# Optimization experiments

Measured on AMD Instinct MI355X. Metric: run time of the kernel, lower is better.

## Reference

```python
import jax, jax.numpy as jnp
import numpy as np
from jax import lax

D = 1024      # d_model
NH = 16       # n_head
CA = 384      # adapter_channels
T = 16        # num_frames
B = 4         # videos
L = 257       # tokens = 16*16 patches + CLS
HW = 16       # spatial side


def setup_inputs() -> dict:
    key = jax.random.key(0)
    ks = jax.random.split(key, 12)
    s = 0.02
    f = lambda k, shp: jax.random.normal(k, shp, jnp.float32) * s
    return {
        'x': jax.random.normal(ks[0], (B * T, L, D), jnp.float32),
        'ln1_g': jnp.ones((D,), jnp.float32), 'ln1_b': jnp.zeros((D,), jnp.float32),
        'w_in': f(ks[1], (3 * D, D)), 'b_in': jnp.zeros((3 * D,), jnp.float32),
        'w_out': f(ks[2], (D, D)), 'b_out': jnp.zeros((D,), jnp.float32),
        'o_fc1_w': f(ks[3], (CA, D)), 'o_fc1_b': jnp.zeros((CA,), jnp.float32),
        'o_conv_w': f(ks[4], (3, 3, 1, CA)), 'o_conv_b': jnp.zeros((CA,), jnp.float32),
        'o_fc2_w': f(ks[5], (D, CA)), 'o_fc2_b': jnp.zeros((D,), jnp.float32),
        'a_fc1_w': f(ks[6], (CA, D)), 'a_fc1_b': jnp.zeros((CA,), jnp.float32),
        'a_conv_w': f(ks[7], (3, 1, CA)), 'a_conv_b': jnp.zeros((CA,), jnp.float32),
        'a_fc2_w': f(ks[8], (D, CA)), 'a_fc2_b': jnp.zeros((D,), jnp.float32),
        'ln2_g': jnp.ones((D,), jnp.float32), 'ln2_b': jnp.zeros((D,), jnp.float32),
        'mlp_fc_w': f(ks[9], (4 * D, D)), 'mlp_fc_b': jnp.zeros((4 * D,), jnp.float32),
        'mlp_proj_w': f(ks[10], (D, 4 * D)), 'mlp_proj_b': jnp.zeros((D,), jnp.float32),
    }


def _ln(x, g, b):
    # fp32 LayerNorm (matches CLIP LayerNorm subclass)
    x32 = x.astype(jnp.float32)
    mu = jnp.mean(x32, -1, keepdims=True)
    var = jnp.mean(jnp.square(x32 - mu), -1, keepdims=True)
    return ((x32 - mu) * lax.rsqrt(var + 1e-5) * g + b).astype(x.dtype)


def _mha(x, w_in, b_in, w_out, b_out):
    BT, Lq, C = x.shape
    hd = C // NH
    qkv = x @ w_in.T + b_in                       # (BT, L, 3C)
    q, k, v = jnp.split(qkv, 3, axis=-1)
    sh = lambda t: t.reshape(BT, Lq, NH, hd).transpose(0, 2, 1, 3)  # (BT, H, L, hd)
    q, k, v = sh(q), sh(k), sh(v)
    scores = jnp.einsum('bhqd,bhkd->bhqk', q * (hd ** -0.5), k)
    attn = jax.nn.softmax(scores, axis=-1)
    out = jnp.einsum('bhqk,bhkd->bhqd', attn, v)
    out = out.transpose(0, 2, 1, 3).reshape(BT, Lq, C)
    return out @ w_out.T + b_out


def _offset_adapter(x, fc1_w, fc1_b, conv_w, conv_b, fc2_w, fc2_b):
    BT, Lx, C = x.shape
    Bv = BT // T
    xs = x[:, 1:, :].reshape(Bv, T, Lx - 1, C)          # drop CLS
    former = jnp.concatenate([xs[:, :1], xs[:, :-1]], axis=1)
    off = xs - former                                    # temporal diff
    off = off @ fc1_w.T + fc1_b                          # (B, T, HW*HW, Ca)
    off = off.reshape(Bv * T, HW, HW, CA)
    # depthwise (1,3,3) Conv3d: kernel size 1 along T -> per-frame 3x3 depthwise conv
    off = lax.conv_general_dilated(off, conv_w, (1, 1), [(1, 1), (1, 1)],
                                   dimension_numbers=('NHWC', 'HWIO', 'NHWC'),
                                   feature_group_count=CA) + conv_b
    off = off.reshape(BT, Lx - 1, CA)
    return off @ fc2_w.T + fc2_b                         # (BT, L-1, C)


def _adapter2(x, a_fc1_w, a_fc1_b, a_conv_w, a_conv_b, a_fc2_w, a_fc2_b,
              o_fc1_w, o_fc1_b, o_conv_w, o_conv_b, o_fc2_w, o_fc2_b):
    BT, Lx, C = x.shape
    Bv = BT // T
    off = _offset_adapter(x, o_fc1_w, o_fc1_b, o_conv_w, o_conv_b, o_fc2_w, o_fc2_b)
    y = x @ a_fc1_w.T + a_fc1_b                          # (BT, L, Ca)
    y = y.reshape(Bv, T, Lx, CA).transpose(0, 2, 1, 3).reshape(Bv * Lx, T, CA)
    # depthwise Conv1d along the temporal axis
    y = lax.conv_general_dilated(y, a_conv_w, (1,), [(1, 1)],
                                 dimension_numbers=('NWC', 'WIO', 'NWC'),
                                 feature_group_count=CA) + a_conv_b
    y = y.reshape(Bv, Lx, T, CA).transpose(0, 2, 1, 3).reshape(BT, Lx, CA)
    y = y @ a_fc2_w.T + a_fc2_b                          # (BT, L, C)
    x_id = x.at[:, 1:, :].add(off)
    return y + x_id


def _block(x, ln1_g, ln1_b, w_in, b_in, w_out, b_out,
           a_fc1_w, a_fc1_b, a_conv_w, a_conv_b, a_fc2_w, a_fc2_b,
           o_fc1_w, o_fc1_b, o_conv_w, o_conv_b, o_fc2_w, o_fc2_b,
           ln2_g, ln2_b, mlp_fc_w, mlp_fc_b, mlp_proj_w, mlp_proj_b):
    x = x + _mha(_ln(x, ln1_g, ln1_b), w_in, b_in, w_out, b_out)
    x = _adapter2(x, a_fc1_w, a_fc1_b, a_conv_w, a_conv_b, a_fc2_w, a_fc2_b,
                  o_fc1_w, o_fc1_b, o_conv_w, o_conv_b, o_fc2_w, o_fc2_b)
    h = _ln(x, ln2_g, ln2_b) @ mlp_fc_w.T + mlp_fc_b
    h = h * jax.nn.sigmoid(1.702 * h)                    # QuickGELU
    return x + h @ mlp_proj_w.T + mlp_proj_b


def reference(x, ln1_g, ln1_b, w_in, b_in, w_out, b_out,
              o_fc1_w, o_fc1_b, o_conv_w, o_conv_b, o_fc2_w, o_fc2_b,
              a_fc1_w, a_fc1_b, a_conv_w, a_conv_b, a_fc2_w, a_fc2_b,
              ln2_g, ln2_b, mlp_fc_w, mlp_fc_b, mlp_proj_w, mlp_proj_b):
    return _block(x, ln1_g, ln1_b, w_in, b_in, w_out, b_out,
                  a_fc1_w, a_fc1_b, a_conv_w, a_conv_b, a_fc2_w, a_fc2_b,
                  o_fc1_w, o_fc1_b, o_conv_w, o_conv_b, o_fc2_w, o_fc2_b,
                  ln2_g, ln2_b, mlp_fc_w, mlp_fc_b, mlp_proj_w, mlp_proj_b)
```

## Files before the change

kernel.cpp:

```cpp
#include <hip/hip_runtime.h>
#include <cstdint>
#include <cstddef>


typedef unsigned short u16;
typedef __attribute__((ext_vector_type(4))) float  f32x4;
typedef __attribute__((ext_vector_type(8))) short  bf16x8;
typedef __attribute__((ext_vector_type(4))) unsigned int u32x4;

#define AS1 __attribute__((address_space(1)))
#define AS3 __attribute__((address_space(3)))

__device__ __forceinline__ float bf2f(u16 u) {
  unsigned int x = ((unsigned int)u) << 16;
  return __builtin_bit_cast(float, x);
}
__device__ __forceinline__ u16 f2bf(float f) {
  unsigned int x = __builtin_bit_cast(unsigned int, f);
  x = x + 0x7fffu + ((x >> 16) & 1u);
  return (u16)(x >> 16);
}
__device__ __forceinline__ unsigned int pack2(float a, float b) {
  return (unsigned int)f2bf(a) | ((unsigned int)f2bf(b) << 16);
}

__device__ __forceinline__ void gload_lds16(const void* g, void* l) {
  __builtin_amdgcn_global_load_lds((const AS1 unsigned int*)g,
                                   (AS3 unsigned int*)l, 16, 0, 0);
}

__global__ __launch_bounds__(256) void cvt_weights(
    const float* __restrict__ w_in, const float* __restrict__ w_out,
    const float* __restrict__ ofc1, const float* __restrict__ ofc2,
    const float* __restrict__ afc1, const float* __restrict__ afc2,
    const float* __restrict__ mfc,  const float* __restrict__ mproj,
    u16* __restrict__ dst)
{
  long i4 = (long)blockIdx.x * 256 + threadIdx.x;
  long e = i4 * 4;
  const float* src; long base;
  if      (e < 3145728L) { src = w_in;  base = 0L; }
  else if (e < 4194304L) { src = w_out; base = 3145728L; }
  else if (e < 4587520L) { src = ofc1;  base = 4194304L; }
  else if (e < 4980736L) { src = ofc2;  base = 4587520L; }
  else if (e < 5373952L) { src = afc1;  base = 4980736L; }
  else if (e < 5767168L) { src = afc2;  base = 5373952L; }
  else if (e < 9961472L) { src = mfc;   base = 5767168L; }
  else                   { src = mproj; base = 9961472L; }
  float4 v = *(const float4*)(src + (e - base));
  uint2 o; o.x = pack2(v.x, v.y); o.y = pack2(v.z, v.w);
  *(uint2*)(dst + e) = o;
}

__global__ __launch_bounds__(256) void ln_bf16(
    const float* __restrict__ x, const float* __restrict__ g,
    const float* __restrict__ b, u16* __restrict__ out)
{
  int row = blockIdx.x;
  const float4* xr = (const float4*)(x + (size_t)row * 1024);
  float4 v = xr[threadIdx.x];
  float s = v.x + v.y + v.z + v.w;
  float q = v.x * v.x + v.y * v.y + v.z * v.z + v.w * v.w;
  #pragma unroll
  for (int m = 1; m < 64; m <<= 1) { s += __shfl_xor(s, m); q += __shfl_xor(q, m); }
  __shared__ float ss[4], qq[4];
  if ((threadIdx.x & 63) == 0) { ss[threadIdx.x >> 6] = s; qq[threadIdx.x >> 6] = q; }
  __syncthreads();
  s = ss[0] + ss[1] + ss[2] + ss[3];
  q = qq[0] + qq[1] + qq[2] + qq[3];
  float mu = s * (1.f / 1024.f);
  float var = q * (1.f / 1024.f) - mu * mu;
  float rs = rsqrtf(var + 1e-5f);
  float4 gg = ((const float4*)g)[threadIdx.x];
  float4 bb = ((const float4*)b)[threadIdx.x];
  float o0 = (v.x - mu) * rs * gg.x + bb.x;
  float o1 = (v.y - mu) * rs * gg.y + bb.y;
  float o2 = (v.z - mu) * rs * gg.z + bb.z;
  float o3 = (v.w - mu) * rs * gg.w + bb.w;
  uint2 o; o.x = pack2(o0, o1); o.y = pack2(o2, o3);
  *(uint2*)(out + (size_t)row * 1024 + threadIdx.x * 4) = o;
}

__global__ __launch_bounds__(256) void diff_bf16(
    const float* __restrict__ x1, u16* __restrict__ out)
{
  int i = blockIdx.x * 256 + threadIdx.x;
  int r = i >> 8;
  int c4 = i & 255;
  int f = r >> 8;
  int p = r & 255;
  int t = f & 15;
  int rowA = f * 257 + 1 + p;
  int rowB = (t == 0) ? rowA : (f - 1) * 257 + 1 + p;
  float4 a = ((const float4*)(x1 + (size_t)rowA * 1024))[c4];
  float4 b = ((const float4*)(x1 + (size_t)rowB * 1024))[c4];
  uint2 o; o.x = pack2(a.x - b.x, a.y - b.y); o.y = pack2(a.z - b.z, a.w - b.w);
  *(uint2*)(out + (size_t)r * 1024 + c4 * 4) = o;
}

__global__ __launch_bounds__(256) void dwconv3x3(
    const u16* __restrict__ in, const float* __restrict__ w,
    const float* __restrict__ bias, u16* __restrict__ out)
{
  int idx = blockIdx.x * 256 + threadIdx.x;
  int c = idx % 384;
  int pos = idx / 384;
  int xx = pos & 15, yy = (pos >> 4) & 15, f = pos >> 8;
  float acc = bias[c];
  #pragma unroll
  for (int kh = 0; kh < 3; kh++) {
    int y2 = yy + kh - 1;
    if (y2 < 0 || y2 > 15) continue;
    #pragma unroll
    for (int kw = 0; kw < 3; kw++) {
      int x2 = xx + kw - 1;
      if (x2 < 0 || x2 > 15) continue;
      acc += bf2f(in[((size_t)(f * 256 + y2 * 16 + x2)) * 384 + c]) * w[(kh * 3 + kw) * 384 + c];
    }
  }
  out[(size_t)idx] = f2bf(acc);
}

__global__ __launch_bounds__(256) void dwconv1d(
    const u16* __restrict__ in, const float* __restrict__ w,
    const float* __restrict__ bias, u16* __restrict__ out)
{
  int idx = blockIdx.x * 256 + threadIdx.x;
  int c = idx % 384;
  int rl = idx / 384;
  int bt = rl / 257, l = rl % 257;
  int bv = bt >> 4, t = bt & 15;
  float acc = bias[c];
  #pragma unroll
  for (int dt = 0; dt < 3; dt++) {
    int tt = t + dt - 1;
    if (tt < 0 || tt > 15) continue;
    acc += bf2f(in[((size_t)((bv * 16 + tt) * 257 + l)) * 384 + c]) * w[dt * 384 + c];
  }
  out[(size_t)idx] = f2bf(acc);
}

enum { EPI_BF16 = 0, EPI_GELU = 1, EPI_RES = 2, EPI_ACC = 3, EPI_ACC_SKIPCLS = 4 };

template <int EPI>
__global__ __launch_bounds__(256) void gemm_bt(
    const u16* __restrict__ A, const u16* __restrict__ B,
    const float* __restrict__ bias,
    float* __restrict__ outF, u16* __restrict__ outB,
    const float* __restrict__ resid,
    int M, int N, int K)
{
  __shared__ u16 As[128 * 64];
  __shared__ u16 Bs[128 * 64];
  const int t = threadIdx.x, l = t & 63, w = t >> 6;
  const int row0 = blockIdx.x * 128, col0 = blockIdx.y * 128;
  const int wr = w >> 1, wc = w & 1;
  const int lo = l & 15, hi = l >> 4;
  const int larow = l >> 3, lacol = (l & 7) * 8;

  f32x4 acc[4][4];
  const f32x4 z = {0.f, 0.f, 0.f, 0.f};
  #pragma unroll
  for (int m = 0; m < 4; m++)
    #pragma unroll
    for (int n = 0; n < 4; n++) acc[m][n] = z;

  for (int k0 = 0; k0 < K; k0 += 64) {
    #pragma unroll
    for (int i = 0; i < 4; i++) {
      int rr = i * 32 + w * 8 + larow;
      int ra = row0 + rr; ra = (ra < M) ? ra : (M - 1);
      gload_lds16(A + (size_t)ra * K + k0 + lacol, As + i * 2048 + w * 512);
      gload_lds16(B + (size_t)(col0 + rr) * K + k0 + lacol, Bs + i * 2048 + w * 512);
    }
    __syncthreads();
    #pragma unroll
    for (int kk = 0; kk < 2; kk++) {
      bf16x8 af[4], bfr[4];
      #pragma unroll
      for (int m = 0; m < 4; m++)
        af[m] = __builtin_bit_cast(bf16x8,
          *(const u32x4*)&As[(wr * 64 + m * 16 + lo) * 64 + kk * 32 + hi * 8]);
      #pragma unroll
      for (int n = 0; n < 4; n++)
        bfr[n] = __builtin_bit_cast(bf16x8,
          *(const u32x4*)&Bs[(wc * 64 + n * 16 + lo) * 64 + kk * 32 + hi * 8]);
      #pragma unroll
      for (int m = 0; m < 4; m++)
        #pragma unroll
        for (int n = 0; n < 4; n++)
          acc[m][n] = __builtin_amdgcn_mfma_f32_16x16x32_bf16(af[m], bfr[n], acc[m][n], 0, 0, 0);
    }
    __syncthreads();
  }

  const int rbase = row0 + wr * 64, cbase = col0 + wc * 64;
  #pragma unroll
  for (int n = 0; n < 4; n++) {
    int colc = cbase + n * 16 + lo;
    float bv = bias[colc];
    #pragma unroll
    for (int m = 0; m < 4; m++) {
      int rr0 = rbase + m * 16 + hi * 4;
      #pragma unroll
      for (int j = 0; j < 4; j++) {
        int r = rr0 + j;
        if (r >= M) continue;
        float v = acc[m][n][j] + bv;
        if constexpr (EPI == EPI_BF16) {
          outB[(size_t)r * N + colc] = f2bf(v);
        } else if constexpr (EPI == EPI_GELU) {
          float gv = v / (1.f + __expf(-1.702f * v));
          outB[(size_t)r * N + colc] = f2bf(gv);
        } else if constexpr (EPI == EPI_RES) {
          float sres = resid[(size_t)r * N + colc] + v;
          outF[(size_t)r * N + colc] = sres;
          outB[(size_t)r * N + colc] = f2bf(sres);
        } else if constexpr (EPI == EPI_ACC) {
          outF[(size_t)r * N + colc] += v;
        } else {
          int rm = (r >> 8) * 257 + (r & 255) + 1;
          outF[(size_t)rm * N + colc] += v;
        }
      }
    }
  }
}

__global__ __launch_bounds__(256) void attn_kernel(
    const u16* __restrict__ qkv, u16* __restrict__ out)
{
  __shared__ u16 Vt[64 * 296];
  __shared__ u16 Ps[4][16 * 136];
  const int bt = blockIdx.x >> 4;
  const int h  = blockIdx.x & 15;
  const int t  = threadIdx.x, l = t & 63, w = t >> 6;
  const int lo = l & 15, hi = l >> 4;
  const size_t base = (size_t)bt * 257 * 3072 + (size_t)h * 64;

  for (int ch = t; ch < 257 * 8; ch += 256) {
    int r = ch >> 3, s8 = ch & 7;
    u32x4 v = *(const u32x4*)(qkv + base + (size_t)r * 3072 + 2048 + s8 * 8);
    union { u32x4 v4; u16 us[8]; } cv; cv.v4 = v;
    #pragma unroll
    for (int i = 0; i < 8; i++) Vt[(s8 * 8 + i) * 296 + r] = cv.us[i];
  }
  for (int ch = t; ch < 64 * 39; ch += 256)
    Vt[(ch / 39) * 296 + 257 + (ch % 39)] = 0;
  __syncthreads();

  for (int c = w; c < 17; c += 4) {
    int qr = c * 16 + lo; qr = (qr < 257) ? qr : 256;
    const u16* qp = qkv + base + (size_t)qr * 3072 + hi * 8;
    bf16x8 q0 = __builtin_bit_cast(bf16x8, *(const u32x4*)qp);
    bf16x8 q1 = __builtin_bit_cast(bf16x8, *(const u32x4*)(qp + 32));

    f32x4 s[17];
    #pragma unroll
    for (int tt = 0; tt < 17; tt++) {
      int kr = tt * 16 + lo; kr = (kr < 257) ? kr : 256;
      const u16* kp = qkv + base + (size_t)kr * 3072 + 1024 + hi * 8;
      bf16x8 k0 = __builtin_bit_cast(bf16x8, *(const u32x4*)kp);
      bf16x8 k1 = __builtin_bit_cast(bf16x8, *(const u32x4*)(kp + 32));
      f32x4 a = {0.f, 0.f, 0.f, 0.f};
      a = __builtin_amdgcn_mfma_f32_16x16x32_bf16(q0, k0, a, 0, 0, 0);
      a = __builtin_amdgcn_mfma_f32_16x16x32_bf16(q1, k1, a, 0, 0, 0);
      s[tt] = a;
    }
    float mx[4] = {-1e30f, -1e30f, -1e30f, -1e30f};
    #pragma unroll
    for (int tt = 0; tt < 17; tt++) {
      int key = tt * 16 + lo;
      #pragma unroll
      for (int j = 0; j < 4; j++) {
        float v = s[tt][j] * 0.125f;
        v = (key < 257) ? v : -1e30f;
        s[tt][j] = v;
        mx[j] = fmaxf(mx[j], v);
      }
    }
    #pragma unroll
    for (int j = 0; j < 4; j++)
      #pragma unroll
      for (int msk = 1; msk < 16; msk <<= 1) mx[j] = fmaxf(mx[j], __shfl_xor(mx[j], msk));
    float sm[4] = {0.f, 0.f, 0.f, 0.f};
    #pragma unroll
    for (int tt = 0; tt < 17; tt++)
      #pragma unroll
      for (int j = 0; j < 4; j++) {
        float p = __expf(s[tt][j] - mx[j]);
        s[tt][j] = p; sm[j] += p;
      }
    #pragma unroll
    for (int j = 0; j < 4; j++) {
      #pragma unroll
      for (int msk = 1; msk < 16; msk <<= 1) sm[j] += __shfl_xor(sm[j], msk);
      sm[j] = 1.f / sm[j];
    }

    u16* P = &Ps[w][0];
    f32x4 o[4];
    #pragma unroll
    for (int n = 0; n < 4; n++) o[n] = (f32x4){0.f, 0.f, 0.f, 0.f};
    #pragma unroll
    for (int ph = 0; ph < 3; ph++) {
      const int TT = (ph < 2) ? 8 : 1;
      #pragma unroll
      for (int ti = 0; ti < TT; ti++) {
        int tt = ph * 8 + ti;
        #pragma unroll
        for (int j = 0; j < 4; j++)
          P[(hi * 4 + j) * 136 + ti * 16 + lo] = f2bf(s[tt][j] * sm[j]);
      }
      if (ph == 2) {
        #pragma unroll
        for (int j = 0; j < 4; j++) P[(hi * 4 + j) * 136 + 16 + lo] = 0;
      }
      const int NKS = (ph < 2) ? 4 : 1;
      #pragma unroll
      for (int ks = 0; ks < NKS; ks++) {
        bf16x8 af = __builtin_bit_cast(bf16x8,
          *(const u32x4*)&P[lo * 136 + ks * 32 + hi * 8]);
        #pragma unroll
        for (int n = 0; n < 4; n++) {
          bf16x8 bfr = __builtin_bit_cast(bf16x8,
            *(const u32x4*)&Vt[(n * 16 + lo) * 296 + ph * 128 + ks * 32 + hi * 8]);
          o[n] = __builtin_amdgcn_mfma_f32_16x16x32_bf16(af, bfr, o[n], 0, 0, 0);
        }
      }
    }
    #pragma unroll
    for (int n = 0; n < 4; n++)
      #pragma unroll
      for (int j = 0; j < 4; j++) {
        int row = c * 16 + hi * 4 + j;
        if (row < 257)
          out[(size_t)(bt * 257 + row) * 1024 + h * 64 + n * 16 + lo] = f2bf(o[n][j]);
      }
  }
}

extern "C" void kernel_launch(void* const* d_in, const int* in_sizes, int n_in,
                              void* d_out, int out_size, void* d_ws, size_t ws_size,
                              hipStream_t stream)
{
  const float* x       = (const float*)d_in[0];
  const float* ln1_g   = (const float*)d_in[1];
  const float* ln1_b   = (const float*)d_in[2];
  const float* w_in    = (const float*)d_in[3];
  const float* b_in    = (const float*)d_in[4];
  const float* w_out   = (const float*)d_in[5];
  const float* b_out   = (const float*)d_in[6];
  const float* o_fc1_w = (const float*)d_in[7];
  const float* o_fc1_b = (const float*)d_in[8];
  const float* o_conv_w= (const float*)d_in[9];
  const float* o_conv_b= (const float*)d_in[10];
  const float* o_fc2_w = (const float*)d_in[11];
  const float* o_fc2_b = (const float*)d_in[12];
  const float* a_fc1_w = (const float*)d_in[13];
  const float* a_fc1_b = (const float*)d_in[14];
  const float* a_conv_w= (const float*)d_in[15];
  const float* a_conv_b= (const float*)d_in[16];
  const float* a_fc2_w = (const float*)d_in[17];
  const float* a_fc2_b = (const float*)d_in[18];
  const float* ln2_g   = (const float*)d_in[19];
  const float* ln2_b   = (const float*)d_in[20];
  const float* mfc_w   = (const float*)d_in[21];
  const float* mfc_b   = (const float*)d_in[22];
  const float* mproj_w = (const float*)d_in[23];
  const float* mproj_b = (const float*)d_in[24];
  float* xo = (float*)d_out;

  char* ws = (char*)d_ws;
  u16* WB = (u16*)ws;
  u16* R0 = (u16*)(ws + 28311552);
  u16* R1 = (u16*)(ws + 28311552 + 33685504);
  u16* R2 = (u16*)(ws + 28311552 + 33685504 + 101056512);
  u16* w_in_bf  = WB + 0;
  u16* w_out_bf = WB + 3145728;
  u16* ofc1_bf  = WB + 4194304;
  u16* ofc2_bf  = WB + 4587520;
  u16* afc1_bf  = WB + 4980736;
  u16* afc2_bf  = WB + 5373952;
  u16* mfc_bf   = WB + 5767168;
  u16* mproj_bf = WB + 9961472;
  u16* off1 = R1;
  u16* offc = R1 + 6291456;
  u16* y1   = R1 + 12582912;
  u16* yc   = R1 + 12582912 + 6316032;

  cvt_weights<<<13824, 256, 0, stream>>>(w_in, w_out, o_fc1_w, o_fc2_w,
                                         a_fc1_w, a_fc2_w, mfc_w, mproj_w, WB);
  ln_bf16<<<16448, 256, 0, stream>>>(x, ln1_g, ln1_b, R0);
  gemm_bt<EPI_BF16><<<dim3(129, 24), 256, 0, stream>>>(
      R0, w_in_bf, b_in, nullptr, R1, nullptr, 16448, 3072, 1024);
  attn_kernel<<<1024, 256, 0, stream>>>(R1, R2);
  gemm_bt<EPI_RES><<<dim3(129, 8), 256, 0, stream>>>(
      R2, w_out_bf, b_out, xo, R0, x, 16448, 1024, 1024);
  diff_bf16<<<16384, 256, 0, stream>>>(xo, R2);
  gemm_bt<EPI_BF16><<<dim3(128, 3), 256, 0, stream>>>(
      R2, ofc1_bf, o_fc1_b, nullptr, off1, nullptr, 16384, 384, 1024);
  dwconv3x3<<<24576, 256, 0, stream>>>(off1, o_conv_w, o_conv_b, offc);
  gemm_bt<EPI_ACC_SKIPCLS><<<dim3(128, 8), 256, 0, stream>>>(
      offc, ofc2_bf, o_fc2_b, xo, nullptr, nullptr, 16384, 1024, 384);
  gemm_bt<EPI_BF16><<<dim3(129, 3), 256, 0, stream>>>(
      R0, afc1_bf, a_fc1_b, nullptr, y1, nullptr, 16448, 384, 1024);
  dwconv1d<<<24672, 256, 0, stream>>>(y1, a_conv_w, a_conv_b, yc);
  gemm_bt<EPI_ACC><<<dim3(129, 8), 256, 0, stream>>>(
      yc, afc2_bf, a_fc2_b, xo, nullptr, nullptr, 16448, 1024, 384);
  ln_bf16<<<16448, 256, 0, stream>>>(xo, ln2_g, ln2_b, R0);
  gemm_bt<EPI_GELU><<<dim3(129, 32), 256, 0, stream>>>(
      R0, mfc_bf, mfc_b, nullptr, R1, nullptr, 16448, 4096, 1024);
  gemm_bt<EPI_ACC><<<dim3(129, 8), 256, 0, stream>>>(
      R1, mproj_bf, mproj_b, xo, nullptr, nullptr, 16448, 1024, 4096);
}
```

Measured before the change: 1.681 ms.

## Add 256x256-tile GEMM with triple-buffered LDS and XCD-aware block remap

Adds a new GEMM kernel with 256x256 output tiles, 512 threads, a three-stage global-to-LDS pipeline using direct LDS loads with an XOR swizzle, and a block-index remap that groups consecutive tiles per XCD. The large N-dimension GEMMs (QKV, out-proj, MLP fc/proj, and the adapter fc2 projections) switch to it. The aim is more operand reuse per tile, better latency hiding and better L2 locality than the old 128-tile kernel. The trade-off is fewer workgroups for the N=1024 GEMMs (260 blocks) and higher register and LDS pressure, which could hurt occupancy or tail balance.

```diff
diff --git a/kernel.cpp b/kernel.cpp
--- a/kernel.cpp
+++ b/kernel.cpp
@@ -23,6 +23,7 @@
 __device__ __forceinline__ unsigned int pack2(float a, float b) {
   return (unsigned int)f2bf(a) | ((unsigned int)f2bf(b) << 16);
 }
+__device__ __forceinline__ int imin(int a, int b) { return a < b ? a : b; }
 
 __device__ __forceinline__ void gload_lds16(const void* g, void* l) {
   __builtin_amdgcn_global_load_lds((const AS1 unsigned int*)g,
@@ -220,6 +221,134 @@
           outF[(size_t)r * N + colc] += v;
         } else {
           int rm = (r >> 8) * 257 + (r & 255) + 1;
+          outF[(size_t)rm * N + colc] += v;
+        }
+      }
+    }
+  }
+}
+
+template <int EPI>
+__global__ __launch_bounds__(512, 2) void gemm256(
+    const u16* __restrict__ A, const u16* __restrict__ B,
+    const float* __restrict__ bias,
+    float* __restrict__ outF, u16* __restrict__ outB,
+    const float* __restrict__ resid,
+    int M, int N, int K, int gm)
+{
+  __shared__ u16 lds[49152];
+  const int tid = threadIdx.x;
+  const int w = tid >> 6, lane = tid & 63;
+  const int lo = lane & 15, hi = lane >> 4;
+  const int wm = w >> 2, wn = w & 3;
+
+  const int nwg = gridDim.x, orig = blockIdx.x;
+  const int q = nwg >> 3, r = nwg & 7;
+  const int xcd = orig & 7, jj = orig >> 3;
+  const int wgid = (xcd < r ? xcd * (q + 1) : r * (q + 1) + (xcd - r) * q) + jj;
+  const int tm = wgid % gm, tn = wgid / gm;
+  const int row0 = tm * 256, col0 = tn * 256;
+
+  const int pr8 = tid >> 3;
+  const int rb  = (((tid & 7) ^ (pr8 & 7)) << 4);
+  const int sr0 = (pr8 << 1) | (rb >> 6);
+  const int scol = (rb & 63) >> 1;
+  const int ar0 = imin(row0 + sr0, M - 1);
+  const int ar1 = imin(row0 + 128 + sr0, M - 1);
+  const u16* aS0 = A + (size_t)ar0 * K + scol;
+  const u16* aS1 = A + (size_t)ar1 * K + scol;
+  const u16* bS0 = B + (size_t)(col0 + sr0) * K + scol;
+  const u16* bS1 = B + (size_t)(col0 + 128 + sr0) * K + scol;
+  u16* ldsA = lds;
+  u16* ldsB = lds + 24576;
+  const int wOff = w * 512;
+
+  auto stage = [&](int b, int kt) {
+    const int k0 = kt << 5;
+    gload_lds16(aS0 + k0, ldsA + b * 8192 + wOff);
+    gload_lds16(aS1 + k0, ldsA + b * 8192 + 4096 + wOff);
+    gload_lds16(bS0 + k0, ldsB + b * 8192 + wOff);
+    gload_lds16(bS1 + k0, ldsB + b * 8192 + 4096 + wOff);
+  };
+
+  const int ax = (((lo & 1) << 5) | (hi << 3)) ^ ((lo >> 1) << 3);
+  const u16* aR = ldsA + (wm * 64 + (lo >> 1)) * 64 + ax;
+  const u16* bR = ldsB + (wn * 32 + (lo >> 1)) * 64 + ax;
+
+  f32x4 acc[8][4];
+  const f32x4 z = {0.f, 0.f, 0.f, 0.f};
+  #pragma unroll
+  for (int m = 0; m < 8; m++)
+    #pragma unroll
+    for (int n = 0; n < 4; n++) acc[m][n] = z;
+
+  auto compute = [&](int b) {
+    const u16* ap = aR + b * 8192;
+    const u16* bp = bR + b * 8192;
+    bf16x8 af[8], bv[4];
+    #pragma unroll
+    for (int n = 0; n < 4; n++)
+      bv[n] = __builtin_bit_cast(bf16x8, *(const u32x4*)(bp + n * 512));
+    #pragma unroll
+    for (int m = 0; m < 8; m++)
+      af[m] = __builtin_bit_cast(bf16x8, *(const u32x4*)(ap + m * 512));
+    #pragma unroll
+    for (int m = 0; m < 8; m++)
+      #pragma unroll
+      for (int n = 0; n < 4; n++)
+        acc[m][n] = __builtin_amdgcn_mfma_f32_16x16x32_bf16(af[m], bv[n], acc[m][n], 0, 0, 0);
+  };
+
+  const int NT = K >> 5;
+  stage(0, 0);
+  stage(1, 1);
+  asm volatile("s_waitcnt vmcnt(4)" ::: "memory");
+  __builtin_amdgcn_s_barrier();
+  asm volatile("" ::: "memory");
+
+  int bcur = 0, bnx2 = 2;
+  for (int t = 0; t < NT - 2; ++t) {
+    stage(bnx2, t + 2);
+    compute(bcur);
+    asm volatile("s_waitcnt vmcnt(4)" ::: "memory");
+    __builtin_amdgcn_s_barrier();
+    asm volatile("" ::: "memory");
+    bcur = (bcur == 2) ? 0 : bcur + 1;
+    bnx2 = (bnx2 == 2) ? 0 : bnx2 + 1;
+  }
+  compute(bcur);
+  asm volatile("s_waitcnt vmcnt(0)" ::: "memory");
+  __builtin_amdgcn_s_barrier();
+  asm volatile("" ::: "memory");
+  bcur = (bcur == 2) ? 0 : bcur + 1;
+  compute(bcur);
+
+  const int rbase = row0 + wm * 128, cbase = col0 + wn * 64;
+  #pragma unroll
+  for (int n = 0; n < 4; n++) {
+    int colc = cbase + n * 16 + lo;
+    float bvv = bias[colc];
+    #pragma unroll
+    for (int m = 0; m < 8; m++) {
+      int rr0 = rbase + m * 16 + hi * 4;
+      #pragma unroll
+      for (int j = 0; j < 4; j++) {
+        int rr = rr0 + j;
+        if (rr >= M) continue;
+        float v = acc[m][n][j] + bvv;
+        if constexpr (EPI == EPI_BF16) {
+          outB[(size_t)rr * N + colc] = f2bf(v);
+        } else if constexpr (EPI == EPI_GELU) {
+          float gv = v / (1.f + __expf(-1.702f * v));
+          outB[(size_t)rr * N + colc] = f2bf(gv);
+        } else if constexpr (EPI == EPI_RES) {
+          float sres = resid[(size_t)rr * N + colc] + v;
+          outF[(size_t)rr * N + colc] = sres;
+          outB[(size_t)rr * N + colc] = f2bf(sres);
+        } else if constexpr (EPI == EPI_ACC) {
+          outF[(size_t)rr * N + colc] += v;
+        } else {
+          int rm = (rr >> 8) * 257 + (rr & 255) + 1;
           outF[(size_t)rm * N + colc] += v;
         }
       }
@@ -392,25 +521,25 @@
   cvt_weights<<<13824, 256, 0, stream>>>(w_in, w_out, o_fc1_w, o_fc2_w,
                                          a_fc1_w, a_fc2_w, mfc_w, mproj_w, WB);
   ln_bf16<<<16448, 256, 0, stream>>>(x, ln1_g, ln1_b, R0);
-  gemm_bt<EPI_BF16><<<dim3(129, 24), 256, 0, stream>>>(
-      R0, w_in_bf, b_in, nullptr, R1, nullptr, 16448, 3072, 1024);
+  gemm256<EPI_BF16><<<65 * 12, 512, 0, stream>>>(
+      R0, w_in_bf, b_in, nullptr, R1, nullptr, 16448, 3072, 1024, 65);
   attn_kernel<<<1024, 256, 0, stream>>>(R1, R2);
-  gemm_bt<EPI_RES><<<dim3(129, 8), 256, 0, stream>>>(
-      R2, w_out_bf, b_out, xo, R0, x, 16448, 1024, 1024);
+  gemm256<EPI_RES><<<65 * 4, 512, 0, stream>>>(
+      R2, w_out_bf, b_out, xo, R0, x, 16448, 1024, 1024, 65);
   diff_bf16<<<16384, 256, 0, stream>>>(xo, R2);
   gemm_bt<EPI_BF16><<<dim3(128, 3), 256, 0, stream>>>(
       R2, ofc1_bf, o_fc1_b, nullptr, off1, nullptr, 16384, 384, 1024);
   dwconv3x3<<<24576, 256, 0, stream>>>(off1, o_conv_w, o_conv_b, offc);
-  gemm_bt<EPI_ACC_SKIPCLS><<<dim3(128, 8), 256, 0, stream>>>(
-      offc, ofc2_bf, o_fc2_b, xo, nullptr, nullptr, 16384, 1024, 384);
+  gemm256<EPI_ACC_SKIPCLS><<<64 * 4, 512, 0, stream>>>(
+      offc, ofc2_bf, o_fc2_b, xo, nullptr, nullptr, 16384, 1024, 384, 64);
   gemm_bt<EPI_BF16><<<dim3(129, 3), 256, 0, stream>>>(
       R0, afc1_bf, a_fc1_b, nullptr, y1, nullptr, 16448, 384, 1024);
   dwconv1d<<<24672, 256, 0, stream>>>(y1, a_conv_w, a_conv_b, yc);
-  gemm_bt<EPI_ACC><<<dim3(129, 8), 256, 0, stream>>>(
-      yc, afc2_bf, a_fc2_b, xo, nullptr, nullptr, 16448, 1024, 384);
+  gemm256<EPI_ACC><<<65 * 4, 512, 0, stream>>>(
+      yc, afc2_bf, a_fc2_b, xo, nullptr, nullptr, 16448, 1024, 384, 65);
   ln_bf16<<<16448, 256, 0, stream>>>(xo, ln2_g, ln2_b, R0);
-  gemm_bt<EPI_GELU><<<dim3(129, 32), 256, 0, stream>>>(
-      R0, mfc_bf, mfc_b, nullptr, R1, nullptr, 16448, 4096, 1024);
-  gemm_bt<EPI_ACC><<<dim3(129, 8), 256, 0, stream>>>(
-      R1, mproj_bf, mproj_b, xo, nullptr, nullptr, 16448, 1024, 4096);
-}
+  gemm256<EPI_GELU><<<65 * 16, 512, 0, stream>>>(
+      R0, mfc_bf, mfc_b, nullptr, R1, nullptr, 16448, 4096, 1024, 65);
+  gemm256<EPI_ACC><<<65 * 4, 512, 0, stream>>>(
+      R1, mproj_bf, mproj_b, xo, nullptr, nullptr, 16448, 1024, 4096, 65);
+}
```

Result: faster. 1.483 ms (-11.7%).
